# Kernel optimization log

Measured on AMD Instinct MI355X. Metric: run time of the kernel, lower is better.

Reference implementation:

```python
import jax, jax.numpy as jnp
import numpy as np
from jax import lax

KSIZE, STRIDE, RATE, SOFTMAX_SCALE = 3, 1, 2, 10.0


def extract_patches(x, k, stride):
    # x: [B,C,H,W] -> [B,C,k,k,oh,ow]; torch-style zero 'same' padding
    B, C, H, W = x.shape
    oh, ow = -(-H // stride), -(-W // stride)
    ph = max(0, (oh - 1) * stride + k - H)
    pw = max(0, (ow - 1) * stride + k - W)
    x = jnp.pad(x, ((0, 0), (0, 0), (ph // 2, ph - ph // 2), (pw // 2, pw - pw // 2)))
    cols = [x[:, :, i:i + (oh - 1) * stride + 1:stride, j:j + (ow - 1) * stride + 1:stride]
            for i in range(k) for j in range(k)]
    return jnp.stack(cols, axis=2).reshape(B, C, k, k, oh, ow)


def setup_inputs():
    key = jax.random.key(0)
    kf, kb = jax.random.split(key)
    f = jax.random.normal(kf, (2, 128, 128, 128), dtype=jnp.float32)
    b = jax.random.normal(kb, (2, 128, 128, 128), dtype=jnp.float32)
    mask = jnp.zeros((2, 1, 512, 512), dtype=jnp.float32)
    mask = mask.at[:, :, 128:384, 128:384].set(1.0)  # central hole: bg patches unavailable
    return {"f": f, "b": b, "mask": mask}


def reference(f, b, mask):
    B, C, H, W = b.shape
    kernel = 2 * RATE
    # raw background patches used for reconstruction (stride = rate*stride)
    raw = extract_patches(b, kernel, RATE * STRIDE)            # [B,C,4,4,Hb,Wb]
    Hb, Wb = raw.shape[-2:]
    L = Hb * Wb
    raw_w = raw.transpose(0, 4, 5, 1, 2, 3).reshape(B, L, C, kernel, kernel)
    # nearest 1/rate downsample (integer rate -> strided slice)
    fs = f[:, :, ::RATE, ::RATE]
    bs = b[:, :, ::RATE, ::RATE]
    Hf, Wf = fs.shape[-2:]
    # matching patches from downsampled background, L2-normalized per patch
    wp = extract_patches(bs, KSIZE, STRIDE)                    # [B,C,3,3,Hb,Wb]
    w = wp.transpose(0, 4, 5, 1, 2, 3).reshape(B, L, C, KSIZE, KSIZE)
    norm = jnp.sqrt(jnp.sum(w * w, axis=(2, 3, 4), keepdims=True))
    w_normed = w / jnp.maximum(norm, 1e-4)
    # mask -> per-patch validity (original uses batch element 0 only)
    ms = mask[:, :, ::4 * RATE, ::4 * RATE]                    # [B,1,Hb,Wb]
    mp = extract_patches(ms, KSIZE, STRIDE)[0]                 # [1,3,3,Hb,Wb]
    mm = (jnp.mean(mp, axis=(0, 1, 2)).reshape(-1) == 0.0).astype(f.dtype)
    mm = mm.reshape(1, L, 1, 1)
    # similarity scores: per-image conv2d of fg with bg patches == patch einsum
    fp = extract_patches(fs, KSIZE, STRIDE)                    # [B,C,3,3,Hf,Wf]
    yi = jnp.einsum('bcpqhw,blcpq->blhw', fp, w_normed)        # [B,L,Hf,Wf]
    yi = yi * mm
    yi = jax.nn.softmax(yi * SOFTMAX_SCALE, axis=1)
    yi = yi * mm
    # argmax offsets relative to reference coordinates (int_bs == int_fs here)
    off = jnp.argmax(yi, axis=1)                               # [B,Hf,Wf]
    h_ref = jnp.arange(Hf)[None, :, None]
    w_ref = jnp.arange(Wf)[None, None, :]
    offsets = jnp.stack([off // Wf - h_ref, off % Wf - w_ref], axis=1)  # [B,2,Hf,Wf]
    # reconstruction: conv_transpose2d(yi, raw_wi, stride=rate, padding=1) / 4
    w_ct = jnp.flip(raw_w.transpose(0, 2, 1, 3, 4), axis=(-2, -1))      # [B,C,L,4,4]
    pad = kernel - 1 - 1  # transpose-conv padding=1 -> conv pad k-1-1
    def ct(a, wk):
        return lax.conv_general_dilated(a[None], wk, (1, 1),
                                        ((pad, pad), (pad, pad)),
                                        lhs_dilation=(RATE, RATE),
                                        dimension_numbers=('NCHW', 'OIHW', 'NCHW'))[0]
    y = jax.vmap(ct)(yi, w_ct) / 4.0                           # [B,C,H,W]
    return y, offsets
```

## Files before the change

kernel.cpp:

```cpp
#include <hip/hip_runtime.h>
#include <hip/hip_bf16.h>
#include <cstdint>

#define B_  2
#define C_  128
#define HH  128
#define WW  128
#define L_  4096
#define K1  1152
#define M2  2048
#define NPAD 3072
#define NCAND 16
#define MARGIN 0.15f
#define PCUT 2e-4f
#define MAXC 512

typedef __attribute__((ext_vector_type(8))) short bf16x8s;
typedef __attribute__((ext_vector_type(4))) float f32x4;
typedef __attribute__((ext_vector_type(2))) float f32x2;
using bf16 = __hip_bfloat16;

__device__ inline float bf16bits2f(unsigned short s) {
  uint32_t u = ((uint32_t)s) << 16;
  return __builtin_bit_cast(float, u);
}
__device__ inline unsigned short f2bf16bits(float x) {
  uint32_t u = __builtin_bit_cast(uint32_t, x);
  u += 0x7fffu + ((u >> 16) & 1u);
  return (unsigned short)(u >> 16);
}

__device__ inline uint8_t fp8_encode(float v) {
  uint32_t s = (__builtin_bit_cast(uint32_t, v) >> 24) & 0x80u;
  float av = fabsf(v);
  uint32_t byte;
  if (av >= 0.015625f) {
    uint32_t bits = __builtin_bit_cast(uint32_t, av);
    uint32_t mant = bits & 0x7fffffu;
    uint32_t E = bits >> 23;
    uint32_t m3 = (mant + 0x7ffffu + ((mant >> 20) & 1u)) >> 20;
    if (m3 == 8u) { m3 = 0u; E++; }
    int e8 = (int)E - 120;
    if (e8 > 15) { e8 = 15; m3 = 6; }
    byte = ((uint32_t)e8 << 3) | m3;
  } else {
    byte = (uint32_t)(av * 512.f + 0.5f);
  }
  return (uint8_t)(s | byte);
}

#if __has_builtin(__builtin_amdgcn_cvt_pk_f32_fp8)
#define FP8PK(d, hi) __builtin_amdgcn_cvt_pk_f32_fp8((d), (hi))
#else
__device__ inline f32x2 FP8PK(uint32_t d, bool hi) {
  uint32_t b0 = hi ? ((d >> 16) & 0xffu) : (d & 0xffu);
  uint32_t b1 = hi ? (d >> 24) : ((d >> 8) & 0xffu);
  f32x2 r;
  r.x = __builtin_bit_cast(float, ((b0 & 0x80u) << 24) | ((b0 & 0x7fu) << 20)) * 0x1p120f;
  r.y = __builtin_bit_cast(float, ((b1 & 0x80u) << 24) | ((b1 & 0x7fu) << 20)) * 0x1p120f;
  return r;
}
#endif

__device__ inline void gload_lds16(const void* g, void* l) {
  auto gp = reinterpret_cast<const __attribute__((address_space(1))) uint32_t*>(
      reinterpret_cast<uintptr_t>(g));
  auto lp = reinterpret_cast<__attribute__((address_space(3))) uint32_t*>(
      reinterpret_cast<uintptr_t>(l));
  __builtin_amdgcn_global_load_lds(gp, lp, 16, 0, 0);
}

__global__ void compute_mm_k(const float* __restrict__ mask, float* __restrict__ mm) {
  int l = blockIdx.x * 256 + threadIdx.x;
  if (l >= L_) return;
  int i = l >> 6, j = l & 63;
  float s = 0.f;
  for (int p = -1; p <= 1; ++p)
    for (int q = -1; q <= 1; ++q) {
      int y = i + p, x = j + q;
      if ((unsigned)y < 64u && (unsigned)x < 64u)
        s += mask[(size_t)(8 * y) * 512 + 8 * x];
    }
  mm[l] = (s == 0.f) ? 1.f : 0.f;
}

__global__ __launch_bounds__(256) void compact_k(const float* __restrict__ mm,
                                                 int* __restrict__ vlist,
                                                 int* __restrict__ vmap,
                                                 int* __restrict__ meta) {
  __shared__ int wpart[4];
  int t = threadIdx.x;
  int lane = t & 63, wid = t >> 6;
  int loc[16];
  int cnt = 0;
#pragma unroll
  for (int s = 0; s < 16; ++s) {
    int l = t * 16 + s;
    loc[s] = cnt;
    cnt += (mm[l] != 0.f) ? 1 : 0;
  }
  int pre = cnt;
#pragma unroll
  for (int o = 1; o < 64; o <<= 1) {
    int u = __shfl_up(pre, o);
    if (lane >= o) pre += u;
  }
  if (lane == 63) wpart[wid] = pre;
  int excl = pre - cnt;
  __syncthreads();
  int base = 0;
  for (int w = 0; w < wid; ++w) base += wpart[w];
  int mybase = base + excl;
#pragma unroll
  for (int s = 0; s < 16; ++s) {
    int l = t * 16 + s;
    if (mm[l] != 0.f) {
      int pos = mybase + loc[s];
      vlist[pos] = l;
      vmap[l] = pos;
    }
  }
  if (t == 0) {
    int total = wpart[0] + wpart[1] + wpart[2] + wpart[3];
    meta[0] = total;
    meta[1] = L_ - total;
  }
}

__global__ __launch_bounds__(256) void prep_u_k(const float* __restrict__ bsrc,
                                                const float* __restrict__ mm,
                                                const int* __restrict__ vmap,
                                                bf16* __restrict__ Ucomp,
                                                float* __restrict__ U32, int bi) {
  __shared__ float red[4];
  int l = blockIdx.x;
  if (mm[l] == 0.f) return;
  int pos = vmap[l];
  int i = l >> 6, j = l & 63;
  int t = threadIdx.x;
  float vals[5];
  float ss = 0.f;
#pragma unroll
  for (int s = 0; s < 5; ++s) {
    int k = t + s * 256;
    float v = 0.f;
    if (k < K1) {
      int c = k / 9, r = k - c * 9;
      int p = r / 3, q = r - p * 3;
      int y = i + p - 1, x = j + q - 1;
      if ((unsigned)y < 64u && (unsigned)x < 64u)
        v = bsrc[(((size_t)bi * C_ + c) * HH + 2 * y) * WW + 2 * x];
    }
    vals[s] = v;
    ss += v * v;
  }
#pragma unroll
  for (int o = 32; o; o >>= 1) ss += __shfl_xor(ss, o);
  if ((t & 63) == 0) red[t >> 6] = ss;
  __syncthreads();
  float tot = red[0] + red[1] + red[2] + red[3];
  float den = fmaxf(sqrtf(tot), 1e-4f);
  float inv = 1.f / den;
  size_t cbase = (size_t)pos * K1;
  size_t obase = (size_t)l * K1;
#pragma unroll
  for (int s = 0; s < 5; ++s) {
    int k = t + s * 256;
    if (k < K1) {
      float u = vals[s] * inv;
      Ucomp[cbase + k] = __float2bfloat16(u);
      U32[obase + k] = u;
    }
  }
}

__global__ __launch_bounds__(256) void prep_fp_k(const float* __restrict__ f,
                                                 bf16* __restrict__ FP,
                                                 float* __restrict__ FP32, int bi) {
  int idx = blockIdx.x * 256 + threadIdx.x;
  if (idx >= L_ * K1) return;
  int hw = idx / K1, k = idx - hw * K1;
  int h = hw >> 6, w = hw & 63;
  int c = k / 9, r = k - c * 9;
  int p = r / 3, q = r - p * 3;
  int y = h + p - 1, x = w + q - 1;
  float v = 0.f;
  if ((unsigned)y < 64u && (unsigned)x < 64u)
    v = f[(((size_t)bi * C_ + c) * HH + 2 * y) * WW + 2 * x];
  FP[(size_t)hw * K1 + k] = __float2bfloat16(v);
  FP32[(size_t)hw * K1 + k] = v;
}

__global__ void prep_bmatT_k(const float* __restrict__ bsrc, uint8_t* __restrict__ BmT8, int bi) {
  int idx = blockIdx.x * 256 + threadIdx.x;
  if (idx >= M2 * L_) return;
  int l = idx >> 11, m = idx & 2047;
  int c = m >> 4, p = (m >> 2) & 3, q = m & 3;
  int i = l >> 6, j = l & 63;
  int y = 2 * i + p - 1, x = 2 * j + q - 1;
  float v = 0.f;
  if ((unsigned)y < 128u && (unsigned)x < 128u)
    v = bsrc[(((size_t)bi * C_ + c) * HH + y) * WW + x];
  BmT8[idx] = fp8_encode(v);
}

__global__ __launch_bounds__(256) void gemm_bt(const bf16* __restrict__ A,
                                               const bf16* __restrict__ B,
                                               bf16* __restrict__ C,
                                               int M, int N, int K) {
  __shared__ __align__(16) bf16 sA[2][128][32];
  __shared__ __align__(16) bf16 sB[2][128][32];
  const int tid = threadIdx.x;
  const int lane = tid & 63;
  const int wid = tid >> 6;
  const int bm = blockIdx.x * 128;
  const int bn = blockIdx.y * 128;
  const int wm = (wid >> 1) * 64;
  const int wn = (wid & 1) * 64;
  const int lrow = lane & 15;
  const int lko = (lane >> 4) * 8;

  f32x4 acc[4][4];
#pragma unroll
  for (int i = 0; i < 4; ++i)
#pragma unroll
    for (int j = 0; j < 4; ++j) acc[i][j] = (f32x4){0.f, 0.f, 0.f, 0.f};

  const int nt = K >> 5;
  const int s0 = tid, s1 = tid + 256;
  const int ar0 = s0 >> 2, ac0 = (s0 & 3) * 8;
  const int ar1 = s1 >> 2, ac1 = (s1 & 3) * 8;

  auto STAGE = [&](int bufi, int t) {
    const int k0 = t * 32;
    gload_lds16(A + (size_t)(bm + ar0) * K + k0 + ac0, &sA[bufi][ar0][ac0]);
    gload_lds16(A + (size_t)(bm + ar1) * K + k0 + ac1, &sA[bufi][ar1][ac1]);
    gload_lds16(B + (size_t)(bn + ar0) * K + k0 + ac0, &sB[bufi][ar0][ac0]);
    gload_lds16(B + (size_t)(bn + ar1) * K + k0 + ac1, &sB[bufi][ar1][ac1]);
  };

  STAGE(0, 0);
  __syncthreads();
  int buf = 0;
  for (int t = 0; t < nt; ++t) {
    if (t + 1 < nt) STAGE(buf ^ 1, t + 1);
    bf16x8s af[4], bfr[4];
#pragma unroll
    for (int fm = 0; fm < 4; ++fm)
      af[fm] = *(const bf16x8s*)&sA[buf][wm + fm * 16 + lrow][lko];
#pragma unroll
    for (int fn = 0; fn < 4; ++fn)
      bfr[fn] = *(const bf16x8s*)&sB[buf][wn + fn * 16 + lrow][lko];
#pragma unroll
    for (int fm = 0; fm < 4; ++fm)
#pragma unroll
      for (int fn = 0; fn < 4; ++fn)
        acc[fm][fn] = __builtin_amdgcn_mfma_f32_16x16x32_bf16(af[fm], bfr[fn], acc[fm][fn], 0, 0, 0);
    __syncthreads();
    buf ^= 1;
  }

  const int crow = (lane >> 4) * 4;
  const int ccol = lane & 15;
#pragma unroll
  for (int fm = 0; fm < 4; ++fm)
#pragma unroll
    for (int fn = 0; fn < 4; ++fn) {
      int r0 = bm + wm + fm * 16 + crow;
      int c0 = bn + wn + fn * 16 + ccol;
#pragma unroll
      for (int r = 0; r < 4; ++r)
        C[(size_t)(r0 + r) * N + c0] = __float2bfloat16(acc[fm][fn][r]);
    }
}

__global__ __launch_bounds__(256) void softmax_spmv_k(const bf16* __restrict__ S,
                                                      const int* __restrict__ vlist,
                                                      const int* __restrict__ meta,
                                                      const uint8_t* __restrict__ BmT8,
                                                      unsigned short* __restrict__ Zt,
                                                      int* __restrict__ cand,
                                                      int* __restrict__ candcnt) {
  __shared__ float rmax[4];
  __shared__ float rsum[4];
  __shared__ int scnt, mcnt;
  __shared__ int slist[MAXC];
  __shared__ float splist[MAXC];
  __shared__ int mlist[NCAND];
  const int row = blockIdx.x;
  const int t = threadIdx.x;
  const int vcnt = meta[0];
  const int nmask = meta[1];
  if (t == 0) { scnt = 0; mcnt = 0; }
  const bool has = (t < NPAD / 16);
  const int c0 = t * 16;
  float xs[16];
#pragma unroll
  for (int s = 0; s < 16; ++s) xs[s] = -1e30f;
  if (has) {
    const bf16* srow = S + (size_t)row * NPAD;
    bf16x8s sv0 = *(const bf16x8s*)&srow[c0];
    bf16x8s sv1 = *(const bf16x8s*)&srow[c0 + 8];
#pragma unroll
    for (int s = 0; s < 8; ++s) {
      xs[s] = bf16bits2f((unsigned short)sv0[s]);
      xs[s + 8] = bf16bits2f((unsigned short)sv1[s]);
    }
  }
  float vmax = -1e30f;
#pragma unroll
  for (int s = 0; s < 16; ++s)
    if (has && c0 + s < vcnt) vmax = fmaxf(vmax, xs[s]);
#pragma unroll
  for (int o = 32; o; o >>= 1) vmax = fmaxf(vmax, __shfl_xor(vmax, o));
  if ((t & 63) == 0) rmax[t >> 6] = vmax;
  __syncthreads();
  vmax = fmaxf(fmaxf(rmax[0], rmax[1]), fmaxf(rmax[2], rmax[3]));
  float gmax = (nmask > 0) ? fmaxf(vmax, 0.f) : vmax;
  float zs = 0.f;
#pragma unroll
  for (int s = 0; s < 16; ++s)
    if (has && c0 + s < vcnt) zs += __expf(10.f * (xs[s] - gmax));
#pragma unroll
  for (int o = 32; o; o >>= 1) zs += __shfl_xor(zs, o);
  if ((t & 63) == 0) rsum[t >> 6] = zs;
  __syncthreads();
  zs = rsum[0] + rsum[1] + rsum[2] + rsum[3] + (float)nmask * __expf(-10.f * gmax);
  float invZ = 1.f / zs;
  float cutx = gmax + __logf(PCUT * zs) * 0.1f;
  if (has) {
#pragma unroll
    for (int s = 0; s < 16; ++s) {
      int c = c0 + s;
      if (c < vcnt) {
        if (xs[s] >= cutx) {
          int pos = atomicAdd(&scnt, 1);
          if (pos < MAXC) {
            slist[pos] = vlist[c];
            splist[pos] = __expf(10.f * (xs[s] - gmax)) * invZ;
          }
        }
        if (xs[s] >= vmax - MARGIN) {
          int pos = atomicAdd(&mcnt, 1);
          if (pos < NCAND) mlist[pos] = vlist[c];
        }
      }
    }
  }
  __syncthreads();
  int nc = min(scnt, MAXC);
  float acc[8] = {0.f, 0.f, 0.f, 0.f, 0.f, 0.f, 0.f, 0.f};
#pragma unroll 4
  for (int ci = 0; ci < nc; ++ci) {
    int l = slist[ci];
    float p = splist[ci];
    const uint32_t* bp = (const uint32_t*)(BmT8 + (size_t)l * M2) + t * 2;
    uint32_t d0 = bp[0], d1 = bp[1];
    f32x2 w0 = FP8PK(d0, false);
    f32x2 w1 = FP8PK(d0, true);
    f32x2 w2 = FP8PK(d1, false);
    f32x2 w3 = FP8PK(d1, true);
    acc[0] += p * w0.x; acc[1] += p * w0.y;
    acc[2] += p * w1.x; acc[3] += p * w1.y;
    acc[4] += p * w2.x; acc[5] += p * w2.y;
    acc[6] += p * w3.x; acc[7] += p * w3.y;
  }
  bf16x8s zv;
#pragma unroll
  for (int j = 0; j < 8; ++j) zv[j] = (short)f2bf16bits(acc[j]);
  *(bf16x8s*)&Zt[(size_t)row * M2 + t * 8] = zv;
  if (t == 0) candcnt[row] = min(mcnt, NCAND);
  if (t < NCAND && t < mcnt) cand[row * NCAND + t] = mlist[t];
}

__global__ __launch_bounds__(256) void transpose_k(const unsigned short* __restrict__ in,
                                                   unsigned short* __restrict__ out) {
  __shared__ ushort2 tile[32][33];
  int bm2 = blockIdx.x * 32;
  int bh = blockIdx.y * 32;
  int tx = threadIdx.x & 31;
  int ty = threadIdx.x >> 5;
  const ushort2* in2 = (const ushort2*)in;
#pragma unroll
  for (int r = 0; r < 32; r += 8)
    tile[ty + r][tx] = in2[(size_t)(bh + ty + r) * (M2 / 2) + bm2 + tx];
  __syncthreads();
#pragma unroll
  for (int r = 0; r < 32; r += 8) {
    ushort2 v = tile[tx][ty + r];
    int mp = bm2 + ty + r;
    out[(size_t)(2 * mp) * L_ + bh + tx] = v.x;
    out[(size_t)(2 * mp + 1) * L_ + bh + tx] = v.y;
  }
}

__global__ __launch_bounds__(256) void rescore_k(const float* __restrict__ FP32,
                                                 const float* __restrict__ U32,
                                                 const int* __restrict__ cand,
                                                 const int* __restrict__ candcnt,
                                                 float* __restrict__ offout, int bi) {
  __shared__ float red[4];
  const int row = blockIdx.x;
  const int t = threadIdx.x;
  const int h = row >> 6, w = row & 63;
  int cnt = candcnt[row];
  int bestl;
  if (cnt <= 1) {
    bestl = cand[row * NCAND];
  } else {
    float fv[5];
#pragma unroll
    for (int s = 0; s < 5; ++s) {
      int k = t + s * 256;
      fv[s] = (k < K1) ? FP32[(size_t)row * K1 + k] : 0.f;
    }
    float bestv = -1e30f;
    bestl = 0x7fffffff;
    for (int ci = 0; ci < cnt; ++ci) {
      int l = cand[row * NCAND + ci];
      const float* urow = U32 + (size_t)l * K1;
      float dot = 0.f;
#pragma unroll
      for (int s = 0; s < 5; ++s) {
        int k = t + s * 256;
        if (k < K1) dot += fv[s] * urow[k];
      }
#pragma unroll
      for (int o = 32; o; o >>= 1) dot += __shfl_xor(dot, o);
      if ((t & 63) == 0) red[t >> 6] = dot;
      __syncthreads();
      dot = red[0] + red[1] + red[2] + red[3];
      if (dot > bestv || (dot == bestv && l < bestl)) { bestv = dot; bestl = l; }
      __syncthreads();
    }
  }
  if (t == 0) {
    int istar = bestl >> 6, jstar = bestl & 63;
    offout[(size_t)bi * 8192 + row] = (float)(istar - h);
    offout[(size_t)bi * 8192 + L_ + row] = (float)(jstar - w);
  }
}

__global__ void gather_k(const unsigned short* __restrict__ Z2, float* __restrict__ yout, int bi) {
  int u = blockIdx.x, c = blockIdx.y;
  int t = threadIdx.x;
  int h0 = (u + 1) >> 1, p0 = (u + 1) & 1;
  int h1 = h0 - 1, p1 = p0 + 2;
  float a0 = 0.f, a1 = 0.f;
#pragma unroll
  for (int e = 0; e < 2; ++e) {
    int h = e ? h1 : h0;
    int p = e ? p1 : p0;
    if ((unsigned)h < 64u) {
      const unsigned short* zb = Z2 + (size_t)(c * 16 + p * 4) * L_ + h * 64;
      a0 += bf16bits2f(zb[1 * L_ + t]);
      if (t >= 1) a0 += bf16bits2f(zb[3 * L_ + (t - 1)]);
      if (t < 63) a1 += bf16bits2f(zb[0 * L_ + (t + 1)]);
      a1 += bf16bits2f(zb[2 * L_ + t]);
    }
  }
  size_t ybase = (((size_t)bi * C_ + c) * HH + u) * WW;
  yout[ybase + 2 * t] = a0 * 0.25f;
  yout[ybase + 2 * t + 1] = a1 * 0.25f;
}

extern "C" void kernel_launch(void* const* d_in, const int* in_sizes, int n_in,
                              void* d_out, int out_size, void* d_ws, size_t ws_size,
                              hipStream_t stream) {
  const float* f = (const float*)d_in[0];
  const float* b = (const float*)d_in[1];
  const float* mask = (const float*)d_in[2];
  float* out = (float*)d_out;
  char* ws = (char*)d_ws;

  size_t off = 0;
  float* mm = (float*)(ws + off);          off += 16384;
  int* vlist = (int*)(ws + off);           off += 16384;
  int* vmap = (int*)(ws + off);            off += 16384;
  int* meta = (int*)(ws + off);            off += 16384;
  int* cand = (int*)(ws + off);            off += (size_t)L_ * NCAND * 4;
  int* candcnt = (int*)(ws + off);         off += 16384;
  bf16* Ucomp = (bf16*)(ws + off);         off += (size_t)NPAD * K1 * 2;
  bf16* FP = (bf16*)(ws + off);            off += (size_t)L_ * K1 * 2;
  float* U32 = (float*)(ws + off);         off += (size_t)L_ * K1 * 4;
  float* FP32 = (float*)(ws + off);        off += (size_t)L_ * K1 * 4;
  uint8_t* BmT8 = (uint8_t*)(ws + off);    off += (size_t)M2 * L_;
  bf16* S = (bf16*)(ws + off);             off += (size_t)L_ * NPAD * 2;
  unsigned short* Zt = (unsigned short*)(ws + off); off += (size_t)M2 * L_ * 2;
  unsigned short* Z2 = (unsigned short*)(ws + off); off += (size_t)M2 * L_ * 2;
  float* yout = out;
  float* offout = out + (size_t)B_ * C_ * HH * WW;

  compute_mm_k<<<16, 256, 0, stream>>>(mask, mm);
  compact_k<<<1, 256, 0, stream>>>(mm, vlist, vmap, meta);
  for (int bi = 0; bi < B_; ++bi) {
    prep_u_k<<<L_, 256, 0, stream>>>(b, mm, vmap, Ucomp, U32, bi);
    prep_fp_k<<<(L_ * K1 + 255) / 256, 256, 0, stream>>>(f, FP, FP32, bi);
    prep_bmatT_k<<<(M2 * L_ + 255) / 256, 256, 0, stream>>>(b, BmT8, bi);
    gemm_bt<<<dim3(32, NPAD / 128), 256, 0, stream>>>(FP, Ucomp, S, L_, NPAD, K1);
    softmax_spmv_k<<<L_, 256, 0, stream>>>(S, vlist, meta, BmT8, Zt, cand, candcnt);
    rescore_k<<<L_, 256, 0, stream>>>(FP32, U32, cand, candcnt, offout, bi);
    transpose_k<<<dim3(M2 / 64, L_ / 32), 256, 0, stream>>>(Zt, Z2);
    gather_k<<<dim3(128, 128), 64, 0, stream>>>(Z2, yout, bi);
  }
}
```

Baseline: 287.6 us.

## Batch both images into single kernel launches and loosen softmax sparsity cutoff

Removes the host loop over the batch. Every kernel now indexes the batch through a grid dimension, and the workspace buffers are sized for both images, so there are half as many launches and each grid is twice as large. The GEMM picks its B matrix per image from the row block index. It also raises the probability cutoff used to pick which entries go into the sparse reconstruction, so fewer candidates are processed. The cost is a larger workspace and a looser approximation of the softmax-weighted sum, which could raise error against the reference.

```diff
diff --git a/kernel.cpp b/kernel.cpp
--- a/kernel.cpp
+++ b/kernel.cpp
@@ -12,7 +12,7 @@
 #define NPAD 3072
 #define NCAND 16
 #define MARGIN 0.15f
-#define PCUT 2e-4f
+#define PCUT 5e-4f
 #define MAXC 512
 
 typedef __attribute__((ext_vector_type(8))) short bf16x8s;
@@ -131,9 +131,10 @@
                                                 const float* __restrict__ mm,
                                                 const int* __restrict__ vmap,
                                                 bf16* __restrict__ Ucomp,
-                                                float* __restrict__ U32, int bi) {
+                                                float* __restrict__ U32) {
   __shared__ float red[4];
   int l = blockIdx.x;
+  int bi = blockIdx.y;
   if (mm[l] == 0.f) return;
   int pos = vmap[l];
   int i = l >> 6, j = l & 63;
@@ -161,8 +162,8 @@
   float tot = red[0] + red[1] + red[2] + red[3];
   float den = fmaxf(sqrtf(tot), 1e-4f);
   float inv = 1.f / den;
-  size_t cbase = (size_t)pos * K1;
-  size_t obase = (size_t)l * K1;
+  size_t cbase = ((size_t)bi * NPAD + pos) * K1;
+  size_t obase = ((size_t)bi * L_ + l) * K1;
 #pragma unroll
   for (int s = 0; s < 5; ++s) {
     int k = t + s * 256;
@@ -176,8 +177,9 @@
 
 __global__ __launch_bounds__(256) void prep_fp_k(const float* __restrict__ f,
                                                  bf16* __restrict__ FP,
-                                                 float* __restrict__ FP32, int bi) {
+                                                 float* __restrict__ FP32) {
   int idx = blockIdx.x * 256 + threadIdx.x;
+  int bi = blockIdx.y;
   if (idx >= L_ * K1) return;
   int hw = idx / K1, k = idx - hw * K1;
   int h = hw >> 6, w = hw & 63;
@@ -187,12 +189,14 @@
   float v = 0.f;
   if ((unsigned)y < 64u && (unsigned)x < 64u)
     v = f[(((size_t)bi * C_ + c) * HH + 2 * y) * WW + 2 * x];
-  FP[(size_t)hw * K1 + k] = __float2bfloat16(v);
-  FP32[(size_t)hw * K1 + k] = v;
-}
-
-__global__ void prep_bmatT_k(const float* __restrict__ bsrc, uint8_t* __restrict__ BmT8, int bi) {
+  size_t o = (size_t)bi * L_ * K1 + idx;
+  FP[o] = __float2bfloat16(v);
+  FP32[o] = v;
+}
+
+__global__ void prep_bmatT_k(const float* __restrict__ bsrc, uint8_t* __restrict__ BmT8) {
   int idx = blockIdx.x * 256 + threadIdx.x;
+  int bi = blockIdx.y;
   if (idx >= M2 * L_) return;
   int l = idx >> 11, m = idx & 2047;
   int c = m >> 4, p = (m >> 2) & 3, q = m & 3;
@@ -201,13 +205,13 @@
   float v = 0.f;
   if ((unsigned)y < 128u && (unsigned)x < 128u)
     v = bsrc[(((size_t)bi * C_ + c) * HH + y) * WW + x];
-  BmT8[idx] = fp8_encode(v);
+  BmT8[(size_t)bi * M2 * L_ + idx] = fp8_encode(v);
 }
 
 __global__ __launch_bounds__(256) void gemm_bt(const bf16* __restrict__ A,
-                                               const bf16* __restrict__ B,
+                                               const bf16* __restrict__ Bbase,
                                                bf16* __restrict__ C,
-                                               int M, int N, int K) {
+                                               int N, int K) {
   __shared__ __align__(16) bf16 sA[2][128][32];
   __shared__ __align__(16) bf16 sB[2][128][32];
   const int tid = threadIdx.x;
@@ -215,6 +219,7 @@
   const int wid = tid >> 6;
   const int bm = blockIdx.x * 128;
   const int bn = blockIdx.y * 128;
+  const bf16* B = Bbase + (size_t)(bm >> 12) * NPAD * K1;
   const int wm = (wid >> 1) * 64;
   const int wn = (wid & 1) * 64;
   const int lrow = lane & 15;
@@ -274,13 +279,13 @@
     }
 }
 
-__global__ __launch_bounds__(256) void softmax_spmv_k(const bf16* __restrict__ S,
+__global__ __launch_bounds__(256) void softmax_spmv_k(const bf16* __restrict__ Sb,
                                                       const int* __restrict__ vlist,
                                                       const int* __restrict__ meta,
-                                                      const uint8_t* __restrict__ BmT8,
-                                                      unsigned short* __restrict__ Zt,
-                                                      int* __restrict__ cand,
-                                                      int* __restrict__ candcnt) {
+                                                      const uint8_t* __restrict__ BmT8b,
+                                                      unsigned short* __restrict__ Ztb,
+                                                      int* __restrict__ candb,
+                                                      int* __restrict__ candcntb) {
   __shared__ float rmax[4];
   __shared__ float rsum[4];
   __shared__ int scnt, mcnt;
@@ -288,9 +293,11 @@
   __shared__ float splist[MAXC];
   __shared__ int mlist[NCAND];
   const int row = blockIdx.x;
+  const int bi = blockIdx.y;
   const int t = threadIdx.x;
   const int vcnt = meta[0];
   const int nmask = meta[1];
+  const uint8_t* BmT8 = BmT8b + (size_t)bi * M2 * L_;
   if (t == 0) { scnt = 0; mcnt = 0; }
   const bool has = (t < NPAD / 16);
   const int c0 = t * 16;
@@ -298,7 +305,7 @@
 #pragma unroll
   for (int s = 0; s < 16; ++s) xs[s] = -1e30f;
   if (has) {
-    const bf16* srow = S + (size_t)row * NPAD;
+    const bf16* srow = Sb + ((size_t)bi * L_ + row) * NPAD;
     bf16x8s sv0 = *(const bf16x8s*)&srow[c0];
     bf16x8s sv1 = *(const bf16x8s*)&srow[c0 + 8];
 #pragma unroll
@@ -368,14 +375,17 @@
   bf16x8s zv;
 #pragma unroll
   for (int j = 0; j < 8; ++j) zv[j] = (short)f2bf16bits(acc[j]);
-  *(bf16x8s*)&Zt[(size_t)row * M2 + t * 8] = zv;
-  if (t == 0) candcnt[row] = min(mcnt, NCAND);
-  if (t < NCAND && t < mcnt) cand[row * NCAND + t] = mlist[t];
-}
-
-__global__ __launch_bounds__(256) void transpose_k(const unsigned short* __restrict__ in,
-                                                   unsigned short* __restrict__ out) {
+  *(bf16x8s*)&Ztb[((size_t)bi * L_ + row) * M2 + t * 8] = zv;
+  if (t == 0) candcntb[bi * L_ + row] = min(mcnt, NCAND);
+  if (t < NCAND && t < mcnt) candb[(bi * L_ + row) * NCAND + t] = mlist[t];
+}
+
+__global__ __launch_bounds__(256) void transpose_k(const unsigned short* __restrict__ inb,
+                                                   unsigned short* __restrict__ outb) {
   __shared__ ushort2 tile[32][33];
+  int bi = blockIdx.z;
+  const unsigned short* in = inb + (size_t)bi * L_ * M2;
+  unsigned short* out = outb + (size_t)bi * M2 * L_;
   int bm2 = blockIdx.x * 32;
   int bh = blockIdx.y * 32;
   int tx = threadIdx.x & 31;
@@ -394,19 +404,23 @@
   }
 }
 
-__global__ __launch_bounds__(256) void rescore_k(const float* __restrict__ FP32,
-                                                 const float* __restrict__ U32,
-                                                 const int* __restrict__ cand,
-                                                 const int* __restrict__ candcnt,
-                                                 float* __restrict__ offout, int bi) {
+__global__ __launch_bounds__(256) void rescore_k(const float* __restrict__ FP32b,
+                                                 const float* __restrict__ U32b,
+                                                 const int* __restrict__ candb,
+                                                 const int* __restrict__ candcntb,
+                                                 float* __restrict__ offout) {
   __shared__ float red[4];
   const int row = blockIdx.x;
+  const int bi = blockIdx.y;
   const int t = threadIdx.x;
   const int h = row >> 6, w = row & 63;
-  int cnt = candcnt[row];
+  const float* FP32 = FP32b + (size_t)bi * L_ * K1;
+  const float* U32 = U32b + (size_t)bi * L_ * K1;
+  const int* cand = candb + (size_t)(bi * L_ + row) * NCAND;
+  int cnt = candcntb[bi * L_ + row];
   int bestl;
   if (cnt <= 1) {
-    bestl = cand[row * NCAND];
+    bestl = cand[0];
   } else {
     float fv[5];
 #pragma unroll
@@ -417,7 +431,7 @@
     float bestv = -1e30f;
     bestl = 0x7fffffff;
     for (int ci = 0; ci < cnt; ++ci) {
-      int l = cand[row * NCAND + ci];
+      int l = cand[ci];
       const float* urow = U32 + (size_t)l * K1;
       float dot = 0.f;
 #pragma unroll
@@ -441,9 +455,10 @@
   }
 }
 
-__global__ void gather_k(const unsigned short* __restrict__ Z2, float* __restrict__ yout, int bi) {
-  int u = blockIdx.x, c = blockIdx.y;
+__global__ void gather_k(const unsigned short* __restrict__ Z2b, float* __restrict__ yout) {
+  int u = blockIdx.x, c = blockIdx.y, bi = blockIdx.z;
   int t = threadIdx.x;
+  const unsigned short* Z2 = Z2b + (size_t)bi * M2 * L_;
   int h0 = (u + 1) >> 1, p0 = (u + 1) & 1;
   int h1 = h0 - 1, p1 = p0 + 2;
   float a0 = 0.f, a1 = 0.f;
@@ -478,29 +493,27 @@
   int* vlist = (int*)(ws + off);           off += 16384;
   int* vmap = (int*)(ws + off);            off += 16384;
   int* meta = (int*)(ws + off);            off += 16384;
-  int* cand = (int*)(ws + off);            off += (size_t)L_ * NCAND * 4;
-  int* candcnt = (int*)(ws + off);         off += 16384;
-  bf16* Ucomp = (bf16*)(ws + off);         off += (size_t)NPAD * K1 * 2;
-  bf16* FP = (bf16*)(ws + off);            off += (size_t)L_ * K1 * 2;
-  float* U32 = (float*)(ws + off);         off += (size_t)L_ * K1 * 4;
-  float* FP32 = (float*)(ws + off);        off += (size_t)L_ * K1 * 4;
-  uint8_t* BmT8 = (uint8_t*)(ws + off);    off += (size_t)M2 * L_;
-  bf16* S = (bf16*)(ws + off);             off += (size_t)L_ * NPAD * 2;
-  unsigned short* Zt = (unsigned short*)(ws + off); off += (size_t)M2 * L_ * 2;
-  unsigned short* Z2 = (unsigned short*)(ws + off); off += (size_t)M2 * L_ * 2;
+  int* cand = (int*)(ws + off);            off += (size_t)B_ * L_ * NCAND * 4;
+  int* candcnt = (int*)(ws + off);         off += 65536;
+  bf16* Ucomp = (bf16*)(ws + off);         off += (size_t)B_ * NPAD * K1 * 2;
+  bf16* FP = (bf16*)(ws + off);            off += (size_t)B_ * L_ * K1 * 2;
+  float* U32 = (float*)(ws + off);         off += (size_t)B_ * L_ * K1 * 4;
+  float* FP32 = (float*)(ws + off);        off += (size_t)B_ * L_ * K1 * 4;
+  uint8_t* BmT8 = (uint8_t*)(ws + off);    off += (size_t)B_ * M2 * L_;
+  bf16* S = (bf16*)(ws + off);             off += (size_t)B_ * L_ * NPAD * 2;
+  unsigned short* Zt = (unsigned short*)(ws + off); off += (size_t)B_ * M2 * L_ * 2;
+  unsigned short* Z2 = (unsigned short*)(ws + off); off += (size_t)B_ * M2 * L_ * 2;
   float* yout = out;
   float* offout = out + (size_t)B_ * C_ * HH * WW;
 
   compute_mm_k<<<16, 256, 0, stream>>>(mask, mm);
   compact_k<<<1, 256, 0, stream>>>(mm, vlist, vmap, meta);
-  for (int bi = 0; bi < B_; ++bi) {
-    prep_u_k<<<L_, 256, 0, stream>>>(b, mm, vmap, Ucomp, U32, bi);
-    prep_fp_k<<<(L_ * K1 + 255) / 256, 256, 0, stream>>>(f, FP, FP32, bi);
-    prep_bmatT_k<<<(M2 * L_ + 255) / 256, 256, 0, stream>>>(b, BmT8, bi);
-    gemm_bt<<<dim3(32, NPAD / 128), 256, 0, stream>>>(FP, Ucomp, S, L_, NPAD, K1);
-    softmax_spmv_k<<<L_, 256, 0, stream>>>(S, vlist, meta, BmT8, Zt, cand, candcnt);
-    rescore_k<<<L_, 256, 0, stream>>>(FP32, U32, cand, candcnt, offout, bi);
-    transpose_k<<<dim3(M2 / 64, L_ / 32), 256, 0, stream>>>(Zt, Z2);
-    gather_k<<<dim3(128, 128), 64, 0, stream>>>(Z2, yout, bi);
-  }
-}
+  prep_u_k<<<dim3(L_, B_), 256, 0, stream>>>(b, mm, vmap, Ucomp, U32);
+  prep_fp_k<<<dim3((L_ * K1 + 255) / 256, B_), 256, 0, stream>>>(f, FP, FP32);
+  prep_bmatT_k<<<dim3((M2 * L_ + 255) / 256, B_), 256, 0, stream>>>(b, BmT8);
+  gemm_bt<<<dim3(B_ * L_ / 128, NPAD / 128), 256, 0, stream>>>(FP, Ucomp, S, NPAD, K1);
+  softmax_spmv_k<<<dim3(L_, B_), 256, 0, stream>>>(S, vlist, meta, BmT8, Zt, cand, candcnt);
+  rescore_k<<<dim3(L_, B_), 256, 0, stream>>>(FP32, U32, cand, candcnt, offout);
+  transpose_k<<<dim3(M2 / 64, L_ / 32, B_), 256, 0, stream>>>(Zt, Z2);
+  gather_k<<<dim3(128, 128, B_), 64, 0, stream>>>(Z2, yout);
+}
```

Result: faster. 256.9 us (-10.7%).
